# Optimization experiments

Hardware: AMD Instinct MI355X
Metric: run time of the kernel (lower is better)

Reference implementation:

```python
import jax, jax.numpy as jnp
import numpy as np

N_NODES = 100000
N_EDGES = 1600000
NEG_SLOPE = 0.2
EPS = 1e-16


def _gat_layer(x, src, dst, W, att_src, att_dst, bias, heads, out_ch):
    # x: [N, F_in]; src/dst: [E'] (self-loops already appended)
    n = x.shape[0]
    h = (x @ W).reshape(n, heads, out_ch)                      # [N, H, C]
    a_src = (h * att_src[None]).sum(-1)                        # [N, H]
    a_dst = (h * att_dst[None]).sum(-1)                        # [N, H]
    e = a_src[src] + a_dst[dst]                                # [E', H]
    e = jnp.where(e > 0, e, NEG_SLOPE * e)                     # leaky_relu
    # segment softmax over incoming edges of each dst node
    m = jax.ops.segment_max(e, dst, num_segments=n)            # [N, H]
    ex = jnp.exp(e - m[dst])                                   # [E', H]
    s = jax.ops.segment_sum(ex, dst, num_segments=n)           # [N, H]
    alpha = ex / (s[dst] + EPS)                                # [E', H]
    msg = h[src] * alpha[:, :, None]                           # [E', H, C]
    out = jax.ops.segment_sum(msg, dst, num_segments=n)        # [N, H, C]
    return out.reshape(n, heads * out_ch) + bias


def setup_inputs() -> dict:
    key = jax.random.key(0)
    ks = jax.random.split(key, 10)
    x = jax.random.normal(ks[0], (N_NODES, 165), dtype=jnp.float32)
    src = jax.random.randint(ks[1], (N_EDGES,), 0, N_NODES, dtype=jnp.int32)
    dst = jax.random.randint(ks[2], (N_EDGES,), 0, N_NODES, dtype=jnp.int32)
    glorot = lambda k, shp: jax.random.normal(k, shp, dtype=jnp.float32) * jnp.sqrt(2.0 / (shp[0] + shp[-1]))
    W1 = glorot(ks[3], (165, 256))
    att_src1 = glorot(ks[4], (4, 64))
    att_dst1 = glorot(ks[5], (4, 64))
    b1 = jnp.zeros((256,), dtype=jnp.float32)
    W2 = glorot(ks[6], (256, 2))
    att_src2 = glorot(ks[7], (1, 2))
    att_dst2 = glorot(ks[8], (1, 2))
    b2 = jnp.zeros((2,), dtype=jnp.float32)
    return {"x": x, "src": src, "dst": dst,
            "W1": W1, "att_src1": att_src1, "att_dst1": att_dst1, "b1": b1,
            "W2": W2, "att_src2": att_src2, "att_dst2": att_dst2, "b2": b2}


def reference(x, src, dst, W1, att_src1, att_dst1, b1, W2, att_src2, att_dst2, b2):
    n = x.shape[0]
    # PyG GATConv adds self-loops by default
    loops = jnp.arange(n, dtype=src.dtype)
    s = jnp.concatenate([src, loops])
    d = jnp.concatenate([dst, loops])
    h = _gat_layer(x, s, d, W1, att_src1, att_dst1, b1, heads=4, out_ch=64)
    h = jax.nn.relu(h)
    # F.dropout with training=False is identity (eval mode)
    out = _gat_layer(h, s, d, W2, att_src2, att_dst2, b2, heads=1, out_ch=2)
    return jax.nn.log_softmax(out, axis=1)
```

## Files before the change

### kernel.cpp

```cpp
#include <hip/hip_runtime.h>
#include <math.h>

#define NN 100000
#define NE 1600000
#define ET (NE + NN)
#define NEG 0.2f
#define KP 192
#define GEMM_BLKS (NN / 32)
#define SLOTS 64
#define NPART 8
#define PART_SZ (NN / NPART)
#define NCHUNK 1024
#define CH ((NE + NCHUNK - 1) / NCHUNK)

typedef __attribute__((ext_vector_type(8))) short short8;
typedef __attribute__((ext_vector_type(4))) float floatx4;

__device__ __forceinline__ unsigned short f2bf(float f) {
    unsigned u = __float_as_uint(f);
    unsigned r = u + 0x7fffu + ((u >> 16) & 1u);
    return (unsigned short)(r >> 16);
}
__device__ __forceinline__ float bflo(unsigned x) { return __uint_as_float(x << 16); }
__device__ __forceinline__ float bfhi(unsigned x) { return __uint_as_float(x & 0xFFFF0000u); }

__global__ __launch_bounds__(256) void k_prep(const float* __restrict__ W,
                                              const float* __restrict__ x,
                                              unsigned short* __restrict__ Wt,
                                              int* __restrict__ deg,
                                              int* __restrict__ esrc,
                                              unsigned* __restrict__ xbf32) {
    const int gid = blockIdx.x * 256 + threadIdx.x;
    const int G = gridDim.x * 256;
    for (int idx = gid; idx < 256 * KP; idx += G) {
        const int n = idx / KP, k = idx - n * KP;
        Wt[idx] = (k < 165) ? f2bf(W[k * 256 + n]) : (unsigned short)0;
    }
    for (int i = gid; i < NN; i += G) { deg[i] = 1; esrc[i << 6] = i; }
    for (int p = gid; p < NN * (KP / 2); p += G) {
        const int n = p / (KP / 2), i = p - n * (KP / 2);
        const int k0 = 2 * i;
        const float v0 = (k0 < 165) ? x[(size_t)n * 165 + k0] : 0.0f;
        const float v1 = (k0 + 1 < 165) ? x[(size_t)n * 165 + k0 + 1] : 0.0f;
        xbf32[p] = (unsigned)f2bf(v0) | ((unsigned)f2bf(v1) << 16);
    }
}

__global__ __launch_bounds__(256) void k_histscat(const int* __restrict__ src,
                                                  const int* __restrict__ dst,
                                                  int* __restrict__ deg,
                                                  int* __restrict__ esrc) {
    const int p = blockIdx.x & 7;
    const int chunk = blockIdx.x >> 3;
    const int e0 = chunk * CH;
    const int e1 = (e0 + CH < NE) ? e0 + CH : NE;
    const int plo = p * PART_SZ, phi = plo + PART_SZ;
    for (int e = e0 + threadIdx.x; e < e1; e += 256) {
        const int d = dst[e];
        if (d >= plo && d < phi) {
            const int s = src[e];
            const int r = atomicAdd(&deg[d], 1);
            if (r < SLOTS) esrc[(d << 6) + r] = s;
        }
    }
}

__global__ __launch_bounds__(256) void k_gemm1(const unsigned short* __restrict__ xbf,
                                               const unsigned short* __restrict__ Wt,
                                               const float* __restrict__ att_s,
                                               const float* __restrict__ att_d,
                                               unsigned short* __restrict__ h1,
                                               float* __restrict__ a_src,
                                               float* __restrict__ a_dst) {
    __shared__ __align__(16) unsigned lds_p[32 * 132];
    const int t = threadIdx.x;
    const int n0 = blockIdx.x * 32;
    const int lane = t & 63, hd = t >> 6;
    const int r16 = lane & 15, quad = lane >> 4;
    floatx4 zero4 = {0.0f, 0.0f, 0.0f, 0.0f};
    floatx4 acc[2][4];
#pragma unroll
    for (int mm = 0; mm < 2; ++mm)
#pragma unroll
        for (int nn = 0; nn < 4; ++nn) acc[mm][nn] = zero4;

    const unsigned short* xr0 = xbf + (size_t)(n0 + r16) * KP;
    const unsigned short* xr1 = xbf + (size_t)(n0 + 16 + r16) * KP;
#pragma unroll
    for (int ks = 0; ks < 6; ++ks) {
        const int kb = ks * 32 + quad * 8;
        short8 a0 = *(const short8*)(xr0 + kb);
        short8 a1 = *(const short8*)(xr1 + kb);
        short8 bf[4];
#pragma unroll
        for (int nn = 0; nn < 4; ++nn)
            bf[nn] = *(const short8*)(Wt + (size_t)(hd * 64 + nn * 16 + r16) * KP + kb);
#pragma unroll
        for (int nn = 0; nn < 4; ++nn) {
            acc[0][nn] = __builtin_amdgcn_mfma_f32_16x16x32_bf16(a0, bf[nn], acc[0][nn], 0, 0, 0);
            acc[1][nn] = __builtin_amdgcn_mfma_f32_16x16x32_bf16(a1, bf[nn], acc[1][nn], 0, 0, 0);
        }
    }

    float asw[4], adw[4];
#pragma unroll
    for (int nn = 0; nn < 4; ++nn) {
        asw[nn] = att_s[hd * 64 + nn * 16 + r16];
        adw[nn] = att_d[hd * 64 + nn * 16 + r16];
    }
#pragma unroll
    for (int mm = 0; mm < 2; ++mm)
#pragma unroll
        for (int r = 0; r < 4; ++r) {
            float ps = acc[mm][0][r] * asw[0] + acc[mm][1][r] * asw[1] +
                       acc[mm][2][r] * asw[2] + acc[mm][3][r] * asw[3];
            float pd = acc[mm][0][r] * adw[0] + acc[mm][1][r] * adw[1] +
                       acc[mm][2][r] * adw[2] + acc[mm][3][r] * adw[3];
            ps += __shfl_xor(ps, 1); ps += __shfl_xor(ps, 2);
            ps += __shfl_xor(ps, 4); ps += __shfl_xor(ps, 8);
            pd += __shfl_xor(pd, 1); pd += __shfl_xor(pd, 2);
            pd += __shfl_xor(pd, 4); pd += __shfl_xor(pd, 8);
            if (r16 == 0) {
                const int node = n0 + mm * 16 + quad * 4 + r;
                a_src[node * 4 + hd] = ps;
                a_dst[node * 4 + hd] = pd;
            }
        }

#pragma unroll
    for (int mm = 0; mm < 2; ++mm)
#pragma unroll
        for (int nn = 0; nn < 4; ++nn)
#pragma unroll
            for (int r = 0; r < 4; ++r) {
                const float v = acc[mm][nn][r];
                const float o = __shfl_xor(v, 1);
                if ((lane & 1) == 0) {
                    const unsigned pk = (unsigned)f2bf(v) | ((unsigned)f2bf(o) << 16);
                    lds_p[(mm * 16 + quad * 4 + r) * 132 + hd * 32 + nn * 8 + (r16 >> 1)] = pk;
                }
            }
    __syncthreads();
    {
        const int row = t & 31, seg = t >> 5;
        const unsigned* p = &lds_p[row * 132 + seg * 16];
        uint4 d0 = *(const uint4*)(p);
        uint4 d1 = *(const uint4*)(p + 4);
        uint4 d2 = *(const uint4*)(p + 8);
        uint4 d3 = *(const uint4*)(p + 12);
        unsigned short* hp = h1 + (size_t)(n0 + row) * 256 + seg * 32;
        *(uint4*)(hp) = d0;
        *(uint4*)(hp + 8) = d1;
        *(uint4*)(hp + 16) = d2;
        *(uint4*)(hp + 24) = d3;
    }
}

__global__ __launch_bounds__(256) void k_l1agg(const unsigned short* __restrict__ h1,
                                               const float* __restrict__ a_src,
                                               const float* __restrict__ a_dst,
                                               const int* __restrict__ deg,
                                               const int* __restrict__ esrc,
                                               const float* __restrict__ b1,
                                               const float* __restrict__ W2,
                                               const float* __restrict__ att_s2,
                                               const float* __restrict__ att_d2,
                                               float4* __restrict__ node2) {
    const int t = threadIdx.x;
    const int n = blockIdx.x * 4 + (t >> 6);
    const int l = t & 63;
    const int q = l >> 4;
    const int sl = l & 15;
    const int head = sl >> 2;
    const int c0 = sl * 16;
    const int el = l >> 2;
    const int hl = l & 3;
    const int dg = deg[n];
    const int ebase = n << 6;
    const float4 ad4 = *(const float4*)&a_dst[n * 4];
    const float adh = (hl == 0) ? ad4.x : (hl == 1) ? ad4.y : (hl == 2) ? ad4.z : ad4.w;

    float ssum = 0.0f;
    float acc[16];
#pragma unroll
    for (int c = 0; c < 16; ++c) acc[c] = 0.0f;

    for (int base = 0; base < dg; base += 16) {
        const int cnt = dg - base;
        const int iters = (cnt < 16) ? cnt : 16;
        int sA = 0; float pA = 0.0f;
        if (el < cnt) {
            sA = esrc[ebase + base + el];
            const float a = a_src[sA * 4 + hl] + adh;
            const float e = (a > 0.0f) ? a : NEG * a;
            pA = __expf(e);
        }
#pragma unroll
        for (int jb = 0; jb < 16; jb += 4) {
            const int j = jb + q;
            const int s = __shfl(sA, j << 2);
            const float p = __shfl(pA, (j << 2) | head);
            if (j < iters) {
                ssum += p;
                const unsigned ho = ((unsigned)s << 8) + c0;
                const uint4 hv0 = *(const uint4*)(h1 + ho);
                const uint4 hv1 = *(const uint4*)(h1 + ho + 8);
                acc[0]  += p * bflo(hv0.x); acc[1]  += p * bfhi(hv0.x);
                acc[2]  += p * bflo(hv0.y); acc[3]  += p * bfhi(hv0.y);
                acc[4]  += p * bflo(hv0.z); acc[5]  += p * bfhi(hv0.z);
                acc[6]  += p * bflo(hv0.w); acc[7]  += p * bfhi(hv0.w);
                acc[8]  += p * bflo(hv1.x); acc[9]  += p * bfhi(hv1.x);
                acc[10] += p * bflo(hv1.y); acc[11] += p * bfhi(hv1.y);
                acc[12] += p * bflo(hv1.z); acc[13] += p * bfhi(hv1.z);
                acc[14] += p * bflo(hv1.w); acc[15] += p * bfhi(hv1.w);
            }
        }
    }
    ssum += __shfl_xor(ssum, 16); ssum += __shfl_xor(ssum, 32);
#pragma unroll
    for (int c = 0; c < 16; ++c) {
        acc[c] += __shfl_xor(acc[c], 16);
        acc[c] += __shfl_xor(acc[c], 32);
    }
    const float inv = 1.0f / ssum;
    float p0 = 0.0f, p1 = 0.0f;
#pragma unroll
    for (int c = 0; c < 16; ++c) {
        const float v = fmaxf(acc[c] * inv + b1[c0 + c], 0.0f);
        p0 += v * W2[(c0 + c) * 2 + 0];
        p1 += v * W2[(c0 + c) * 2 + 1];
    }
    if (q) { p0 = 0.0f; p1 = 0.0f; }
#pragma unroll
    for (int off = 32; off; off >>= 1) {
        p0 += __shfl_down(p0, off);
        p1 += __shfl_down(p1, off);
    }
    if (l == 0) {
        const float as2v = p0 * att_s2[0] + p1 * att_s2[1];
        const float ad2v = p0 * att_d2[0] + p1 * att_d2[1];
        node2[n] = make_float4(p0, p1, as2v, ad2v);
    }
}

__global__ __launch_bounds__(256) void k_l2agg(const float4* __restrict__ node2,
                                               const int* __restrict__ deg,
                                               const int* __restrict__ esrc,
                                               const float* __restrict__ b2,
                                               float* __restrict__ out) {
    const int t = threadIdx.x;
    const int l = t & 63;
    const int g = l >> 4;
    const int i = l & 15;
    const int n = blockIdx.x * 16 + (t >> 6) * 4 + g;
    const int dg = deg[n];
    const int ebase = n << 6;
    const float adst = node2[n].w;
    float ssum = 0.0f, a0 = 0.0f, a1 = 0.0f;
    for (int idx = i; idx < dg; idx += 16) {
        const int s = esrc[ebase + idx];
        const float4 r = node2[s];
        const float a = r.z + adst;
        const float e = (a > 0.0f) ? a : NEG * a;
        const float p = __expf(e);
        ssum += p; a0 += p * r.x; a1 += p * r.y;
    }
#pragma unroll
    for (int off = 8; off; off >>= 1) {
        ssum += __shfl_xor(ssum, off);
        a0 += __shfl_xor(a0, off);
        a1 += __shfl_xor(a1, off);
    }
    if (i == 0) {
        const float inv = 1.0f / ssum;
        const float z0 = a0 * inv + b2[0];
        const float z1 = a1 * inv + b2[1];
        const float mz = fmaxf(z0, z1);
        const float lse = mz + __logf(__expf(z0 - mz) + __expf(z1 - mz));
        out[n * 2 + 0] = z0 - lse;
        out[n * 2 + 1] = z1 - lse;
    }
}

extern "C" void kernel_launch(void* const* d_in, const int* in_sizes, int n_in,
                              void* d_out, int out_size, void* d_ws, size_t ws_size,
                              hipStream_t stream) {
    const float* x    = (const float*)d_in[0];
    const int*   src  = (const int*)d_in[1];
    const int*   dst  = (const int*)d_in[2];
    const float* W1   = (const float*)d_in[3];
    const float* as1w = (const float*)d_in[4];
    const float* ad1w = (const float*)d_in[5];
    const float* b1   = (const float*)d_in[6];
    const float* W2   = (const float*)d_in[7];
    const float* as2w = (const float*)d_in[8];
    const float* ad2w = (const float*)d_in[9];
    const float* b2   = (const float*)d_in[10];
    float* out = (float*)d_out;

    char* w = (char*)d_ws;
    unsigned short* h1  = (unsigned short*)w; w += (size_t)NN * 256 * 2;
    unsigned short* Wt  = (unsigned short*)w; w += (size_t)256 * KP * 2;
    unsigned short* xbf = (unsigned short*)w; w += (size_t)NN * KP * 2;
    float* a_src = (float*)w; w += (size_t)NN * 4 * 4;
    float* a_dst = (float*)w; w += (size_t)NN * 4 * 4;
    float4* node2 = (float4*)w; w += (size_t)NN * 4 * 4;
    int* deg     = (int*)w;   w += (size_t)NN * 4;
    int* esrc    = (int*)w;   w += (size_t)NN * SLOTS * 4;

    k_prep<<<2048, 256, 0, stream>>>(W1, x, Wt, deg, esrc, (unsigned*)xbf);
    k_histscat<<<NCHUNK * NPART, 256, 0, stream>>>(src, dst, deg, esrc);
    k_gemm1<<<GEMM_BLKS, 256, 0, stream>>>(xbf, Wt, as1w, ad1w, h1, a_src, a_dst);
    k_l1agg<<<NN / 4, 256, 0, stream>>>(h1, a_src, a_dst, deg, esrc, b1, W2, as2w, ad2w, node2);
    k_l2agg<<<NN / 16, 256, 0, stream>>>(node2, deg, esrc, b2, out);
}
```

Before: 447.9 us.

## Merge five kernels into one cooperative persistent kernel with grid syncs

Folds the prep, edge bucketing, GEMM, layer-1 aggregation and layer-2 aggregation kernels into a single cooperative kernel. Each stage runs as a grid-stride loop over the original block indices, and stages are separated by grid.sync(). The goal is to remove the per-launch overhead and inter-kernel gaps of the five separate launches. In exchange, occupancy is capped by the launch-bounds hint and the grid size is hardcoded to 256 CUs times the occupancy. The persistent loops may also lose the latency hiding that the previous oversubscribed grids provided.

```diff
diff --git a/kernel.cpp b/kernel.cpp
--- a/kernel.cpp
+++ b/kernel.cpp
@@ -1,5 +1,8 @@
 #include <hip/hip_runtime.h>
+#include <hip/hip_cooperative_groups.h>
 #include <math.h>
+
+namespace cg = cooperative_groups;
 
 #define NN 100000
 #define NE 1600000
@@ -24,261 +27,262 @@
 __device__ __forceinline__ float bflo(unsigned x) { return __uint_as_float(x << 16); }
 __device__ __forceinline__ float bfhi(unsigned x) { return __uint_as_float(x & 0xFFFF0000u); }
 
-__global__ __launch_bounds__(256) void k_prep(const float* __restrict__ W,
-                                              const float* __restrict__ x,
-                                              unsigned short* __restrict__ Wt,
-                                              int* __restrict__ deg,
-                                              int* __restrict__ esrc,
-                                              unsigned* __restrict__ xbf32) {
-    const int gid = blockIdx.x * 256 + threadIdx.x;
-    const int G = gridDim.x * 256;
-    for (int idx = gid; idx < 256 * KP; idx += G) {
-        const int n = idx / KP, k = idx - n * KP;
-        Wt[idx] = (k < 165) ? f2bf(W[k * 256 + n]) : (unsigned short)0;
-    }
-    for (int i = gid; i < NN; i += G) { deg[i] = 1; esrc[i << 6] = i; }
-    for (int p = gid; p < NN * (KP / 2); p += G) {
-        const int n = p / (KP / 2), i = p - n * (KP / 2);
-        const int k0 = 2 * i;
-        const float v0 = (k0 < 165) ? x[(size_t)n * 165 + k0] : 0.0f;
-        const float v1 = (k0 + 1 < 165) ? x[(size_t)n * 165 + k0 + 1] : 0.0f;
-        xbf32[p] = (unsigned)f2bf(v0) | ((unsigned)f2bf(v1) << 16);
-    }
-}
-
-__global__ __launch_bounds__(256) void k_histscat(const int* __restrict__ src,
-                                                  const int* __restrict__ dst,
-                                                  int* __restrict__ deg,
-                                                  int* __restrict__ esrc) {
-    const int p = blockIdx.x & 7;
-    const int chunk = blockIdx.x >> 3;
-    const int e0 = chunk * CH;
-    const int e1 = (e0 + CH < NE) ? e0 + CH : NE;
-    const int plo = p * PART_SZ, phi = plo + PART_SZ;
-    for (int e = e0 + threadIdx.x; e < e1; e += 256) {
-        const int d = dst[e];
-        if (d >= plo && d < phi) {
-            const int s = src[e];
-            const int r = atomicAdd(&deg[d], 1);
-            if (r < SLOTS) esrc[(d << 6) + r] = s;
-        }
-    }
-}
-
-__global__ __launch_bounds__(256) void k_gemm1(const unsigned short* __restrict__ xbf,
-                                               const unsigned short* __restrict__ Wt,
-                                               const float* __restrict__ att_s,
-                                               const float* __restrict__ att_d,
-                                               unsigned short* __restrict__ h1,
-                                               float* __restrict__ a_src,
-                                               float* __restrict__ a_dst) {
+__global__ __launch_bounds__(256, 6) void k_mega(
+    const float* __restrict__ W1, const float* __restrict__ x,
+    const int* __restrict__ src, const int* __restrict__ dst,
+    const float* __restrict__ as1, const float* __restrict__ ad1,
+    const float* __restrict__ b1, const float* __restrict__ W2,
+    const float* __restrict__ as2, const float* __restrict__ ad2,
+    const float* __restrict__ b2,
+    unsigned short* __restrict__ Wt, unsigned* __restrict__ xbf32,
+    int* __restrict__ deg, int* __restrict__ esrc,
+    unsigned short* __restrict__ h1, float* __restrict__ a_src,
+    float* __restrict__ a_dst, float4* __restrict__ node2,
+    float* __restrict__ out)
+{
     __shared__ __align__(16) unsigned lds_p[32 * 132];
+    cg::grid_group grid = cg::this_grid();
     const int t = threadIdx.x;
-    const int n0 = blockIdx.x * 32;
-    const int lane = t & 63, hd = t >> 6;
-    const int r16 = lane & 15, quad = lane >> 4;
-    floatx4 zero4 = {0.0f, 0.0f, 0.0f, 0.0f};
-    floatx4 acc[2][4];
-#pragma unroll
-    for (int mm = 0; mm < 2; ++mm)
-#pragma unroll
-        for (int nn = 0; nn < 4; ++nn) acc[mm][nn] = zero4;
-
-    const unsigned short* xr0 = xbf + (size_t)(n0 + r16) * KP;
-    const unsigned short* xr1 = xbf + (size_t)(n0 + 16 + r16) * KP;
-#pragma unroll
-    for (int ks = 0; ks < 6; ++ks) {
-        const int kb = ks * 32 + quad * 8;
-        short8 a0 = *(const short8*)(xr0 + kb);
-        short8 a1 = *(const short8*)(xr1 + kb);
-        short8 bf[4];
-#pragma unroll
-        for (int nn = 0; nn < 4; ++nn)
-            bf[nn] = *(const short8*)(Wt + (size_t)(hd * 64 + nn * 16 + r16) * KP + kb);
+
+    {
+        const int gid = blockIdx.x * 256 + t;
+        const int G = gridDim.x * 256;
+        for (int idx = gid; idx < 256 * KP; idx += G) {
+            const int n = idx / KP, k = idx - n * KP;
+            Wt[idx] = (k < 165) ? f2bf(W1[k * 256 + n]) : (unsigned short)0;
+        }
+        for (int i = gid; i < NN; i += G) { deg[i] = 1; esrc[i << 6] = i; }
+        for (int p = gid; p < NN * (KP / 2); p += G) {
+            const int n = p / (KP / 2), i = p - n * (KP / 2);
+            const int k0 = 2 * i;
+            const float v0 = (k0 < 165) ? x[(size_t)n * 165 + k0] : 0.0f;
+            const float v1 = (k0 + 1 < 165) ? x[(size_t)n * 165 + k0 + 1] : 0.0f;
+            xbf32[p] = (unsigned)f2bf(v0) | ((unsigned)f2bf(v1) << 16);
+        }
+    }
+    grid.sync();
+
+    {
+        for (int b = blockIdx.x; b < NPART * NCHUNK; b += gridDim.x) {
+            const int p = b & 7;
+            const int chunk = b >> 3;
+            const int e0 = chunk * CH;
+            const int e1 = (e0 + CH < NE) ? e0 + CH : NE;
+            const int plo = p * PART_SZ, phi = plo + PART_SZ;
+            for (int e = e0 + t; e < e1; e += 256) {
+                const int d = dst[e];
+                if (d >= plo && d < phi) {
+                    const int s = src[e];
+                    const int r = atomicAdd(&deg[d], 1);
+                    if (r < SLOTS) esrc[(d << 6) + r] = s;
+                }
+            }
+        }
+    }
+    grid.sync();
+
+    {
+        const unsigned short* xbf = (const unsigned short*)xbf32;
+        const int lane = t & 63, hd = t >> 6;
+        const int r16 = lane & 15, quad = lane >> 4;
+        float asw[4], adw[4];
 #pragma unroll
         for (int nn = 0; nn < 4; ++nn) {
-            acc[0][nn] = __builtin_amdgcn_mfma_f32_16x16x32_bf16(a0, bf[nn], acc[0][nn], 0, 0, 0);
-            acc[1][nn] = __builtin_amdgcn_mfma_f32_16x16x32_bf16(a1, bf[nn], acc[1][nn], 0, 0, 0);
-        }
-    }
-
-    float asw[4], adw[4];
-#pragma unroll
-    for (int nn = 0; nn < 4; ++nn) {
-        asw[nn] = att_s[hd * 64 + nn * 16 + r16];
-        adw[nn] = att_d[hd * 64 + nn * 16 + r16];
-    }
-#pragma unroll
-    for (int mm = 0; mm < 2; ++mm)
-#pragma unroll
-        for (int r = 0; r < 4; ++r) {
-            float ps = acc[mm][0][r] * asw[0] + acc[mm][1][r] * asw[1] +
-                       acc[mm][2][r] * asw[2] + acc[mm][3][r] * asw[3];
-            float pd = acc[mm][0][r] * adw[0] + acc[mm][1][r] * adw[1] +
-                       acc[mm][2][r] * adw[2] + acc[mm][3][r] * adw[3];
-            ps += __shfl_xor(ps, 1); ps += __shfl_xor(ps, 2);
-            ps += __shfl_xor(ps, 4); ps += __shfl_xor(ps, 8);
-            pd += __shfl_xor(pd, 1); pd += __shfl_xor(pd, 2);
-            pd += __shfl_xor(pd, 4); pd += __shfl_xor(pd, 8);
-            if (r16 == 0) {
-                const int node = n0 + mm * 16 + quad * 4 + r;
-                a_src[node * 4 + hd] = ps;
-                a_dst[node * 4 + hd] = pd;
-            }
-        }
-
-#pragma unroll
-    for (int mm = 0; mm < 2; ++mm)
-#pragma unroll
-        for (int nn = 0; nn < 4; ++nn)
-#pragma unroll
-            for (int r = 0; r < 4; ++r) {
-                const float v = acc[mm][nn][r];
-                const float o = __shfl_xor(v, 1);
-                if ((lane & 1) == 0) {
-                    const unsigned pk = (unsigned)f2bf(v) | ((unsigned)f2bf(o) << 16);
-                    lds_p[(mm * 16 + quad * 4 + r) * 132 + hd * 32 + nn * 8 + (r16 >> 1)] = pk;
-                }
-            }
-    __syncthreads();
-    {
-        const int row = t & 31, seg = t >> 5;
-        const unsigned* p = &lds_p[row * 132 + seg * 16];
-        uint4 d0 = *(const uint4*)(p);
-        uint4 d1 = *(const uint4*)(p + 4);
-        uint4 d2 = *(const uint4*)(p + 8);
-        uint4 d3 = *(const uint4*)(p + 12);
-        unsigned short* hp = h1 + (size_t)(n0 + row) * 256 + seg * 32;
-        *(uint4*)(hp) = d0;
-        *(uint4*)(hp + 8) = d1;
-        *(uint4*)(hp + 16) = d2;
-        *(uint4*)(hp + 24) = d3;
-    }
-}
-
-__global__ __launch_bounds__(256) void k_l1agg(const unsigned short* __restrict__ h1,
-                                               const float* __restrict__ a_src,
-                                               const float* __restrict__ a_dst,
-                                               const int* __restrict__ deg,
-                                               const int* __restrict__ esrc,
-                                               const float* __restrict__ b1,
-                                               const float* __restrict__ W2,
-                                               const float* __restrict__ att_s2,
-                                               const float* __restrict__ att_d2,
-                                               float4* __restrict__ node2) {
-    const int t = threadIdx.x;
-    const int n = blockIdx.x * 4 + (t >> 6);
-    const int l = t & 63;
-    const int q = l >> 4;
-    const int sl = l & 15;
-    const int head = sl >> 2;
-    const int c0 = sl * 16;
-    const int el = l >> 2;
-    const int hl = l & 3;
-    const int dg = deg[n];
-    const int ebase = n << 6;
-    const float4 ad4 = *(const float4*)&a_dst[n * 4];
-    const float adh = (hl == 0) ? ad4.x : (hl == 1) ? ad4.y : (hl == 2) ? ad4.z : ad4.w;
-
-    float ssum = 0.0f;
-    float acc[16];
-#pragma unroll
-    for (int c = 0; c < 16; ++c) acc[c] = 0.0f;
-
-    for (int base = 0; base < dg; base += 16) {
-        const int cnt = dg - base;
-        const int iters = (cnt < 16) ? cnt : 16;
-        int sA = 0; float pA = 0.0f;
-        if (el < cnt) {
-            sA = esrc[ebase + base + el];
-            const float a = a_src[sA * 4 + hl] + adh;
-            const float e = (a > 0.0f) ? a : NEG * a;
-            pA = __expf(e);
-        }
-#pragma unroll
-        for (int jb = 0; jb < 16; jb += 4) {
-            const int j = jb + q;
-            const int s = __shfl(sA, j << 2);
-            const float p = __shfl(pA, (j << 2) | head);
-            if (j < iters) {
-                ssum += p;
-                const unsigned ho = ((unsigned)s << 8) + c0;
-                const uint4 hv0 = *(const uint4*)(h1 + ho);
-                const uint4 hv1 = *(const uint4*)(h1 + ho + 8);
-                acc[0]  += p * bflo(hv0.x); acc[1]  += p * bfhi(hv0.x);
-                acc[2]  += p * bflo(hv0.y); acc[3]  += p * bfhi(hv0.y);
-                acc[4]  += p * bflo(hv0.z); acc[5]  += p * bfhi(hv0.z);
-                acc[6]  += p * bflo(hv0.w); acc[7]  += p * bfhi(hv0.w);
-                acc[8]  += p * bflo(hv1.x); acc[9]  += p * bfhi(hv1.x);
-                acc[10] += p * bflo(hv1.y); acc[11] += p * bfhi(hv1.y);
-                acc[12] += p * bflo(hv1.z); acc[13] += p * bfhi(hv1.z);
-                acc[14] += p * bflo(hv1.w); acc[15] += p * bfhi(hv1.w);
-            }
-        }
-    }
-    ssum += __shfl_xor(ssum, 16); ssum += __shfl_xor(ssum, 32);
-#pragma unroll
-    for (int c = 0; c < 16; ++c) {
-        acc[c] += __shfl_xor(acc[c], 16);
-        acc[c] += __shfl_xor(acc[c], 32);
-    }
-    const float inv = 1.0f / ssum;
-    float p0 = 0.0f, p1 = 0.0f;
-#pragma unroll
-    for (int c = 0; c < 16; ++c) {
-        const float v = fmaxf(acc[c] * inv + b1[c0 + c], 0.0f);
-        p0 += v * W2[(c0 + c) * 2 + 0];
-        p1 += v * W2[(c0 + c) * 2 + 1];
-    }
-    if (q) { p0 = 0.0f; p1 = 0.0f; }
-#pragma unroll
-    for (int off = 32; off; off >>= 1) {
-        p0 += __shfl_down(p0, off);
-        p1 += __shfl_down(p1, off);
-    }
-    if (l == 0) {
-        const float as2v = p0 * att_s2[0] + p1 * att_s2[1];
-        const float ad2v = p0 * att_d2[0] + p1 * att_d2[1];
-        node2[n] = make_float4(p0, p1, as2v, ad2v);
-    }
-}
-
-__global__ __launch_bounds__(256) void k_l2agg(const float4* __restrict__ node2,
-                                               const int* __restrict__ deg,
-                                               const int* __restrict__ esrc,
-                                               const float* __restrict__ b2,
-                                               float* __restrict__ out) {
-    const int t = threadIdx.x;
-    const int l = t & 63;
-    const int g = l >> 4;
-    const int i = l & 15;
-    const int n = blockIdx.x * 16 + (t >> 6) * 4 + g;
-    const int dg = deg[n];
-    const int ebase = n << 6;
-    const float adst = node2[n].w;
-    float ssum = 0.0f, a0 = 0.0f, a1 = 0.0f;
-    for (int idx = i; idx < dg; idx += 16) {
-        const int s = esrc[ebase + idx];
-        const float4 r = node2[s];
-        const float a = r.z + adst;
-        const float e = (a > 0.0f) ? a : NEG * a;
-        const float p = __expf(e);
-        ssum += p; a0 += p * r.x; a1 += p * r.y;
-    }
-#pragma unroll
-    for (int off = 8; off; off >>= 1) {
-        ssum += __shfl_xor(ssum, off);
-        a0 += __shfl_xor(a0, off);
-        a1 += __shfl_xor(a1, off);
-    }
-    if (i == 0) {
-        const float inv = 1.0f / ssum;
-        const float z0 = a0 * inv + b2[0];
-        const float z1 = a1 * inv + b2[1];
-        const float mz = fmaxf(z0, z1);
-        const float lse = mz + __logf(__expf(z0 - mz) + __expf(z1 - mz));
-        out[n * 2 + 0] = z0 - lse;
-        out[n * 2 + 1] = z1 - lse;
+            asw[nn] = as1[hd * 64 + nn * 16 + r16];
+            adw[nn] = ad1[hd * 64 + nn * 16 + r16];
+        }
+        for (int tb = blockIdx.x; tb < GEMM_BLKS; tb += gridDim.x) {
+            __syncthreads();
+            const int n0 = tb * 32;
+            floatx4 zero4 = {0.0f, 0.0f, 0.0f, 0.0f};
+            floatx4 acc[2][4];
+#pragma unroll
+            for (int mm = 0; mm < 2; ++mm)
+#pragma unroll
+                for (int nn = 0; nn < 4; ++nn) acc[mm][nn] = zero4;
+
+            const unsigned short* xr0 = xbf + (size_t)(n0 + r16) * KP;
+            const unsigned short* xr1 = xbf + (size_t)(n0 + 16 + r16) * KP;
+#pragma unroll
+            for (int ks = 0; ks < 6; ++ks) {
+                const int kb = ks * 32 + quad * 8;
+                short8 a0 = *(const short8*)(xr0 + kb);
+                short8 a1 = *(const short8*)(xr1 + kb);
+                short8 bfv[4];
+#pragma unroll
+                for (int nn = 0; nn < 4; ++nn)
+                    bfv[nn] = *(const short8*)(Wt + (size_t)(hd * 64 + nn * 16 + r16) * KP + kb);
+#pragma unroll
+                for (int nn = 0; nn < 4; ++nn) {
+                    acc[0][nn] = __builtin_amdgcn_mfma_f32_16x16x32_bf16(a0, bfv[nn], acc[0][nn], 0, 0, 0);
+                    acc[1][nn] = __builtin_amdgcn_mfma_f32_16x16x32_bf16(a1, bfv[nn], acc[1][nn], 0, 0, 0);
+                }
+            }
+
+#pragma unroll
+            for (int mm = 0; mm < 2; ++mm)
+#pragma unroll
+                for (int r = 0; r < 4; ++r) {
+                    float ps = acc[mm][0][r] * asw[0] + acc[mm][1][r] * asw[1] +
+                               acc[mm][2][r] * asw[2] + acc[mm][3][r] * asw[3];
+                    float pd = acc[mm][0][r] * adw[0] + acc[mm][1][r] * adw[1] +
+                               acc[mm][2][r] * adw[2] + acc[mm][3][r] * adw[3];
+                    ps += __shfl_xor(ps, 1); ps += __shfl_xor(ps, 2);
+                    ps += __shfl_xor(ps, 4); ps += __shfl_xor(ps, 8);
+                    pd += __shfl_xor(pd, 1); pd += __shfl_xor(pd, 2);
+                    pd += __shfl_xor(pd, 4); pd += __shfl_xor(pd, 8);
+                    if (r16 == 0) {
+                        const int node = n0 + mm * 16 + quad * 4 + r;
+                        a_src[node * 4 + hd] = ps;
+                        a_dst[node * 4 + hd] = pd;
+                    }
+                }
+
+#pragma unroll
+            for (int mm = 0; mm < 2; ++mm)
+#pragma unroll
+                for (int nn = 0; nn < 4; ++nn)
+#pragma unroll
+                    for (int r = 0; r < 4; ++r) {
+                        const float v = acc[mm][nn][r];
+                        const float o = __shfl_xor(v, 1);
+                        if ((lane & 1) == 0) {
+                            const unsigned pk = (unsigned)f2bf(v) | ((unsigned)f2bf(o) << 16);
+                            lds_p[(mm * 16 + quad * 4 + r) * 132 + hd * 32 + nn * 8 + (r16 >> 1)] = pk;
+                        }
+                    }
+            __syncthreads();
+            {
+                const int row = t & 31, seg = t >> 5;
+                const unsigned* p = &lds_p[row * 132 + seg * 16];
+                uint4 d0 = *(const uint4*)(p);
+                uint4 d1 = *(const uint4*)(p + 4);
+                uint4 d2 = *(const uint4*)(p + 8);
+                uint4 d3 = *(const uint4*)(p + 12);
+                unsigned short* hp = h1 + (size_t)(n0 + row) * 256 + seg * 32;
+                *(uint4*)(hp) = d0;
+                *(uint4*)(hp + 8) = d1;
+                *(uint4*)(hp + 16) = d2;
+                *(uint4*)(hp + 24) = d3;
+            }
+        }
+    }
+    grid.sync();
+
+    {
+        const int l = t & 63;
+        const int q = l >> 4;
+        const int sl = l & 15;
+        const int head = sl >> 2;
+        const int c0 = sl * 16;
+        const int el = l >> 2;
+        const int hl = l & 3;
+        for (int nb = blockIdx.x; nb < NN / 4; nb += gridDim.x) {
+            const int n = nb * 4 + (t >> 6);
+            const int dg = deg[n];
+            const int ebase = n << 6;
+            const float4 ad4 = *(const float4*)&a_dst[n * 4];
+            const float adh = (hl == 0) ? ad4.x : (hl == 1) ? ad4.y : (hl == 2) ? ad4.z : ad4.w;
+
+            float ssum = 0.0f;
+            float acc[16];
+#pragma unroll
+            for (int c = 0; c < 16; ++c) acc[c] = 0.0f;
+
+            for (int base = 0; base < dg; base += 16) {
+                const int cnt = dg - base;
+                const int iters = (cnt < 16) ? cnt : 16;
+                int sA = 0; float pA = 0.0f;
+                if (el < cnt) {
+                    sA = esrc[ebase + base + el];
+                    const float a = a_src[sA * 4 + hl] + adh;
+                    const float e = (a > 0.0f) ? a : NEG * a;
+                    pA = __expf(e);
+                }
+#pragma unroll
+                for (int jb = 0; jb < 16; jb += 4) {
+                    const int j = jb + q;
+                    const int s = __shfl(sA, j << 2);
+                    const float p = __shfl(pA, (j << 2) | head);
+                    if (j < iters) {
+                        ssum += p;
+                        const unsigned ho = ((unsigned)s << 8) + c0;
+                        const uint4 hv0 = *(const uint4*)(h1 + ho);
+                        const uint4 hv1 = *(const uint4*)(h1 + ho + 8);
+                        acc[0]  += p * bflo(hv0.x); acc[1]  += p * bfhi(hv0.x);
+                        acc[2]  += p * bflo(hv0.y); acc[3]  += p * bfhi(hv0.y);
+                        acc[4]  += p * bflo(hv0.z); acc[5]  += p * bfhi(hv0.z);
+                        acc[6]  += p * bflo(hv0.w); acc[7]  += p * bfhi(hv0.w);
+                        acc[8]  += p * bflo(hv1.x); acc[9]  += p * bfhi(hv1.x);
+                        acc[10] += p * bflo(hv1.y); acc[11] += p * bfhi(hv1.y);
+                        acc[12] += p * bflo(hv1.z); acc[13] += p * bfhi(hv1.z);
+                        acc[14] += p * bflo(hv1.w); acc[15] += p * bfhi(hv1.w);
+                    }
+                }
+            }
+            ssum += __shfl_xor(ssum, 16); ssum += __shfl_xor(ssum, 32);
+#pragma unroll
+            for (int c = 0; c < 16; ++c) {
+                acc[c] += __shfl_xor(acc[c], 16);
+                acc[c] += __shfl_xor(acc[c], 32);
+            }
+            const float inv = 1.0f / ssum;
+            float p0 = 0.0f, p1 = 0.0f;
+#pragma unroll
+            for (int c = 0; c < 16; ++c) {
+                const float v = fmaxf(acc[c] * inv + b1[c0 + c], 0.0f);
+                p0 += v * W2[(c0 + c) * 2 + 0];
+                p1 += v * W2[(c0 + c) * 2 + 1];
+            }
+            if (q) { p0 = 0.0f; p1 = 0.0f; }
+#pragma unroll
+            for (int off = 32; off; off >>= 1) {
+                p0 += __shfl_down(p0, off);
+                p1 += __shfl_down(p1, off);
+            }
+            if (l == 0) {
+                const float as2v = p0 * as2[0] + p1 * as2[1];
+                const float ad2v = p0 * ad2[0] + p1 * ad2[1];
+                node2[n] = make_float4(p0, p1, as2v, ad2v);
+            }
+        }
+    }
+    grid.sync();
+
+    {
+        const int l = t & 63;
+        const int g = l >> 4;
+        const int i = l & 15;
+        for (int nb = blockIdx.x; nb < NN / 16; nb += gridDim.x) {
+            const int n = nb * 16 + (t >> 6) * 4 + g;
+            const int dg = deg[n];
+            const int ebase = n << 6;
+            const float adst = node2[n].w;
+            float ssum = 0.0f, a0 = 0.0f, a1 = 0.0f;
+            for (int idx = i; idx < dg; idx += 16) {
+                const int s = esrc[ebase + idx];
+                const float4 r = node2[s];
+                const float a = r.z + adst;
+                const float e = (a > 0.0f) ? a : NEG * a;
+                const float p = __expf(e);
+                ssum += p; a0 += p * r.x; a1 += p * r.y;
+            }
+#pragma unroll
+            for (int off = 8; off; off >>= 1) {
+                ssum += __shfl_xor(ssum, off);
+                a0 += __shfl_xor(a0, off);
+                a1 += __shfl_xor(a1, off);
+            }
+            if (i == 0) {
+                const float inv = 1.0f / ssum;
+                const float z0 = a0 * inv + b2[0];
+                const float z1 = a1 * inv + b2[1];
+                const float mz = fmaxf(z0, z1);
+                const float lse = mz + __logf(__expf(z0 - mz) + __expf(z1 - mz));
+                out[n * 2 + 0] = z0 - lse;
+                out[n * 2 + 1] = z1 - lse;
+            }
+        }
     }
 }
 
@@ -301,16 +305,24 @@
     char* w = (char*)d_ws;
     unsigned short* h1  = (unsigned short*)w; w += (size_t)NN * 256 * 2;
     unsigned short* Wt  = (unsigned short*)w; w += (size_t)256 * KP * 2;
-    unsigned short* xbf = (unsigned short*)w; w += (size_t)NN * KP * 2;
+    unsigned* xbf32     = (unsigned*)w;       w += (size_t)NN * KP * 2;
     float* a_src = (float*)w; w += (size_t)NN * 4 * 4;
     float* a_dst = (float*)w; w += (size_t)NN * 4 * 4;
     float4* node2 = (float4*)w; w += (size_t)NN * 4 * 4;
     int* deg     = (int*)w;   w += (size_t)NN * 4;
     int* esrc    = (int*)w;   w += (size_t)NN * SLOTS * 4;
 
-    k_prep<<<2048, 256, 0, stream>>>(W1, x, Wt, deg, esrc, (unsigned*)xbf);
-    k_histscat<<<NCHUNK * NPART, 256, 0, stream>>>(src, dst, deg, esrc);
-    k_gemm1<<<GEMM_BLKS, 256, 0, stream>>>(xbf, Wt, as1w, ad1w, h1, a_src, a_dst);
-    k_l1agg<<<NN / 4, 256, 0, stream>>>(h1, a_src, a_dst, deg, esrc, b1, W2, as2w, ad2w, node2);
-    k_l2agg<<<NN / 16, 256, 0, stream>>>(node2, deg, esrc, b2, out);
+    int maxb = 0;
+    (void)hipOccupancyMaxActiveBlocksPerMultiprocessor(&maxb, (const void*)k_mega, 256, 0);
+    if (maxb < 1) maxb = 1;
+    if (maxb > 8) maxb = 8;
+    dim3 grid(256 * maxb);
+
+    void* args[] = {
+        (void*)&W1, (void*)&x, (void*)&src, (void*)&dst,
+        (void*)&as1w, (void*)&ad1w, (void*)&b1, (void*)&W2,
+        (void*)&as2w, (void*)&ad2w, (void*)&b2,
+        (void*)&Wt, (void*)&xbf32, (void*)&deg, (void*)&esrc,
+        (void*)&h1, (void*)&a_src, (void*)&a_dst, (void*)&node2, (void*)&out };
+    hipLaunchCooperativeKernel((void*)k_mega, grid, dim3(256), args, 0, stream);
 }
```

Result: slower. 1.024 ms (+128.5%).

## Fuse edge bucketing with layer-1 GEMM and convert x to bf16 in LDS

Applied to the files above, without the earlier changes.

Merges the histogram/scatter kernel and the layer-1 GEMM into one launch. The first block range buckets edges by destination and the remaining blocks compute the GEMM. Each GEMM block now converts its 32 rows of x from fp32 to bf16 straight into LDS, so the separate bf16 copy of x in global memory is no longer written or read. This removes a global round-trip and a kernel launch, and lets the atomic-heavy scatter overlap with MFMA work. The cost is an LDS staging step with strided fp32 loads, which may have bank conflicts, plus an extra barrier before LDS is reused for output.

```diff
diff --git a/kernel.cpp b/kernel.cpp
--- a/kernel.cpp
+++ b/kernel.cpp
@@ -12,6 +12,8 @@
 #define PART_SZ (NN / NPART)
 #define NCHUNK 1024
 #define CH ((NE + NCHUNK - 1) / NCHUNK)
+#define HS_BLKS (NPART * NCHUNK)
+#define LDA 200
 
 typedef __attribute__((ext_vector_type(8))) short short8;
 typedef __attribute__((ext_vector_type(4))) float floatx4;
@@ -25,11 +27,9 @@
 __device__ __forceinline__ float bfhi(unsigned x) { return __uint_as_float(x & 0xFFFF0000u); }
 
 __global__ __launch_bounds__(256) void k_prep(const float* __restrict__ W,
-                                              const float* __restrict__ x,
                                               unsigned short* __restrict__ Wt,
                                               int* __restrict__ deg,
-                                              int* __restrict__ esrc,
-                                              unsigned* __restrict__ xbf32) {
+                                              int* __restrict__ esrc) {
     const int gid = blockIdx.x * 256 + threadIdx.x;
     const int G = gridDim.x * 256;
     for (int idx = gid; idx < 256 * KP; idx += G) {
@@ -37,44 +37,53 @@
         Wt[idx] = (k < 165) ? f2bf(W[k * 256 + n]) : (unsigned short)0;
     }
     for (int i = gid; i < NN; i += G) { deg[i] = 1; esrc[i << 6] = i; }
-    for (int p = gid; p < NN * (KP / 2); p += G) {
-        const int n = p / (KP / 2), i = p - n * (KP / 2);
-        const int k0 = 2 * i;
-        const float v0 = (k0 < 165) ? x[(size_t)n * 165 + k0] : 0.0f;
-        const float v1 = (k0 + 1 < 165) ? x[(size_t)n * 165 + k0 + 1] : 0.0f;
-        xbf32[p] = (unsigned)f2bf(v0) | ((unsigned)f2bf(v1) << 16);
-    }
-}
-
-__global__ __launch_bounds__(256) void k_histscat(const int* __restrict__ src,
-                                                  const int* __restrict__ dst,
-                                                  int* __restrict__ deg,
-                                                  int* __restrict__ esrc) {
-    const int p = blockIdx.x & 7;
-    const int chunk = blockIdx.x >> 3;
-    const int e0 = chunk * CH;
-    const int e1 = (e0 + CH < NE) ? e0 + CH : NE;
-    const int plo = p * PART_SZ, phi = plo + PART_SZ;
-    for (int e = e0 + threadIdx.x; e < e1; e += 256) {
-        const int d = dst[e];
-        if (d >= plo && d < phi) {
-            const int s = src[e];
-            const int r = atomicAdd(&deg[d], 1);
-            if (r < SLOTS) esrc[(d << 6) + r] = s;
-        }
-    }
-}
-
-__global__ __launch_bounds__(256) void k_gemm1(const unsigned short* __restrict__ xbf,
-                                               const unsigned short* __restrict__ Wt,
-                                               const float* __restrict__ att_s,
-                                               const float* __restrict__ att_d,
-                                               unsigned short* __restrict__ h1,
-                                               float* __restrict__ a_src,
-                                               float* __restrict__ a_dst) {
-    __shared__ __align__(16) unsigned lds_p[32 * 132];
+}
+
+__global__ __launch_bounds__(256) void k_hsgemm(const int* __restrict__ src,
+                                                const int* __restrict__ dst,
+                                                const float* __restrict__ x,
+                                                const unsigned short* __restrict__ Wt,
+                                                const float* __restrict__ att_s,
+                                                const float* __restrict__ att_d,
+                                                int* __restrict__ deg,
+                                                int* __restrict__ esrc,
+                                                unsigned short* __restrict__ h1,
+                                                float* __restrict__ a_src,
+                                                float* __restrict__ a_dst) {
+    __shared__ __align__(16) unsigned lds_u32[32 * 132];
     const int t = threadIdx.x;
-    const int n0 = blockIdx.x * 32;
+    const int b = blockIdx.x;
+
+    if (b < HS_BLKS) {
+        const int p = b & 7;
+        const int chunk = b >> 3;
+        const int e0 = chunk * CH;
+        const int e1 = (e0 + CH < NE) ? e0 + CH : NE;
+        const int plo = p * PART_SZ, phi = plo + PART_SZ;
+        for (int e = e0 + t; e < e1; e += 256) {
+            const int d = dst[e];
+            if (d >= plo && d < phi) {
+                const int s = src[e];
+                const int r = atomicAdd(&deg[d], 1);
+                if (r < SLOTS) esrc[(d << 6) + r] = s;
+            }
+        }
+        return;
+    }
+
+    const int n0 = (b - HS_BLKS) * 32;
+    unsigned short* lds_a = (unsigned short*)lds_u32;
+
+    for (int i = t; i < 32 * 165; i += 256) {
+        const int n = i / 165, k = i - n * 165;
+        lds_a[n * LDA + k] = f2bf(x[(size_t)(n0 + n) * 165 + k]);
+    }
+    for (int i = t; i < 32 * (LDA - 165); i += 256) {
+        const int n = i / (LDA - 165), k = 165 + (i - n * (LDA - 165));
+        lds_a[n * LDA + k] = 0;
+    }
+    __syncthreads();
+
     const int lane = t & 63, hd = t >> 6;
     const int r16 = lane & 15, quad = lane >> 4;
     floatx4 zero4 = {0.0f, 0.0f, 0.0f, 0.0f};
@@ -84,21 +93,21 @@
 #pragma unroll
         for (int nn = 0; nn < 4; ++nn) acc[mm][nn] = zero4;
 
-    const unsigned short* xr0 = xbf + (size_t)(n0 + r16) * KP;
-    const unsigned short* xr1 = xbf + (size_t)(n0 + 16 + r16) * KP;
+    const unsigned short* ar0 = lds_a + r16 * LDA;
+    const unsigned short* ar1 = lds_a + (16 + r16) * LDA;
 #pragma unroll
     for (int ks = 0; ks < 6; ++ks) {
         const int kb = ks * 32 + quad * 8;
-        short8 a0 = *(const short8*)(xr0 + kb);
-        short8 a1 = *(const short8*)(xr1 + kb);
-        short8 bf[4];
+        short8 a0 = *(const short8*)(ar0 + kb);
+        short8 a1 = *(const short8*)(ar1 + kb);
+        short8 bfv[4];
 #pragma unroll
         for (int nn = 0; nn < 4; ++nn)
-            bf[nn] = *(const short8*)(Wt + (size_t)(hd * 64 + nn * 16 + r16) * KP + kb);
+            bfv[nn] = *(const short8*)(Wt + (size_t)(hd * 64 + nn * 16 + r16) * KP + kb);
 #pragma unroll
         for (int nn = 0; nn < 4; ++nn) {
-            acc[0][nn] = __builtin_amdgcn_mfma_f32_16x16x32_bf16(a0, bf[nn], acc[0][nn], 0, 0, 0);
-            acc[1][nn] = __builtin_amdgcn_mfma_f32_16x16x32_bf16(a1, bf[nn], acc[1][nn], 0, 0, 0);
+            acc[0][nn] = __builtin_amdgcn_mfma_f32_16x16x32_bf16(a0, bfv[nn], acc[0][nn], 0, 0, 0);
+            acc[1][nn] = __builtin_amdgcn_mfma_f32_16x16x32_bf16(a1, bfv[nn], acc[1][nn], 0, 0, 0);
         }
     }
 
@@ -127,6 +136,7 @@
             }
         }
 
+    __syncthreads();
 #pragma unroll
     for (int mm = 0; mm < 2; ++mm)
 #pragma unroll
@@ -137,13 +147,13 @@
                 const float o = __shfl_xor(v, 1);
                 if ((lane & 1) == 0) {
                     const unsigned pk = (unsigned)f2bf(v) | ((unsigned)f2bf(o) << 16);
-                    lds_p[(mm * 16 + quad * 4 + r) * 132 + hd * 32 + nn * 8 + (r16 >> 1)] = pk;
+                    lds_u32[(mm * 16 + quad * 4 + r) * 132 + hd * 32 + nn * 8 + (r16 >> 1)] = pk;
                 }
             }
     __syncthreads();
     {
         const int row = t & 31, seg = t >> 5;
-        const unsigned* p = &lds_p[row * 132 + seg * 16];
+        const unsigned* p = &lds_u32[row * 132 + seg * 16];
         uint4 d0 = *(const uint4*)(p);
         uint4 d1 = *(const uint4*)(p + 4);
         uint4 d2 = *(const uint4*)(p + 8);
@@ -301,16 +311,15 @@
     char* w = (char*)d_ws;
     unsigned short* h1  = (unsigned short*)w; w += (size_t)NN * 256 * 2;
     unsigned short* Wt  = (unsigned short*)w; w += (size_t)256 * KP * 2;
-    unsigned short* xbf = (unsigned short*)w; w += (size_t)NN * KP * 2;
     float* a_src = (float*)w; w += (size_t)NN * 4 * 4;
     float* a_dst = (float*)w; w += (size_t)NN * 4 * 4;
     float4* node2 = (float4*)w; w += (size_t)NN * 4 * 4;
     int* deg     = (int*)w;   w += (size_t)NN * 4;
     int* esrc    = (int*)w;   w += (size_t)NN * SLOTS * 4;
 
-    k_prep<<<2048, 256, 0, stream>>>(W1, x, Wt, deg, esrc, (unsigned*)xbf);
-    k_histscat<<<NCHUNK * NPART, 256, 0, stream>>>(src, dst, deg, esrc);
-    k_gemm1<<<GEMM_BLKS, 256, 0, stream>>>(xbf, Wt, as1w, ad1w, h1, a_src, a_dst);
+    k_prep<<<512, 256, 0, stream>>>(W1, Wt, deg, esrc);
+    k_hsgemm<<<HS_BLKS + GEMM_BLKS, 256, 0, stream>>>(src, dst, x, Wt, as1w, ad1w,
+                                                      deg, esrc, h1, a_src, a_dst);
     k_l1agg<<<NN / 4, 256, 0, stream>>>(h1, a_src, a_dst, deg, esrc, b1, W2, as2w, ad2w, node2);
     k_l2agg<<<NN / 16, 256, 0, stream>>>(node2, deg, esrc, b2, out);
 }
```

Measured after the change: 424.5 us. -5.2%, faster.
